# Kernel tuning notes

Hardware: AMD Instinct MI355X
Metric: run time of the kernel (lower is better)

## Reference

```python
import jax, jax.numpy as jnp
import numpy as np

D = 1024      # query_dim
H = 16        # heads
DH = 64       # dim_head
I = H * DH    # inner_dim = 1024
DC = 768      # context_dim
FF = 4 * D    # ff inner dim = 4096
EPS = 1e-5
SCALE = DH ** -0.5


def setup_inputs() -> dict:
    key = jax.random.key(0)
    ks = jax.random.split(key, 20)
    s = 0.02
    inp = {
        'x': jax.random.normal(ks[0], (2, 2048, D), jnp.float32),
        'context': jax.random.normal(ks[1], (2, 77, DC), jnp.float32),
        'ln1_g': jnp.ones((D,), jnp.float32), 'ln1_b': jnp.zeros((D,), jnp.float32),
        'ln2_g': jnp.ones((D,), jnp.float32), 'ln2_b': jnp.zeros((D,), jnp.float32),
        'ln3_g': jnp.ones((D,), jnp.float32), 'ln3_b': jnp.zeros((D,), jnp.float32),
        'Wq1': jax.random.normal(ks[2], (D, I), jnp.float32) * s,
        'Wk1': jax.random.normal(ks[3], (D, I), jnp.float32) * s,
        'Wv1': jax.random.normal(ks[4], (D, I), jnp.float32) * s,
        'Wo1': jax.random.normal(ks[5], (I, D), jnp.float32) * s,
        'bo1': jnp.zeros((D,), jnp.float32),
        'Wq2': jax.random.normal(ks[6], (D, I), jnp.float32) * s,
        'Wk2': jax.random.normal(ks[7], (DC, I), jnp.float32) * s,
        'Wv2': jax.random.normal(ks[8], (DC, I), jnp.float32) * s,
        'Wo2': jax.random.normal(ks[9], (I, D), jnp.float32) * s,
        'bo2': jnp.zeros((D,), jnp.float32),
        'Wff1': jax.random.normal(ks[10], (D, 2 * FF), jnp.float32) * s,
        'bff1': jnp.zeros((2 * FF,), jnp.float32),
        'Wff2': jax.random.normal(ks[11], (FF, D), jnp.float32) * s,
        'bff2': jnp.zeros((D,), jnp.float32),
    }
    return inp


def layer_norm(x, g, b):
    m = jnp.mean(x, axis=-1, keepdims=True)
    v = jnp.mean(jnp.square(x - m), axis=-1, keepdims=True)
    return (x - m) * jax.lax.rsqrt(v + EPS) * g + b


def cross_attention(x, ctx, Wq, Wk, Wv, Wo, bo):
    # x: [B,N,D], ctx: [B,M,Dc]
    B, N, _ = x.shape
    M = ctx.shape[1]
    q = (x @ Wq).reshape(B, N, H, DH).transpose(0, 2, 1, 3)    # [B,H,N,DH]
    k = (ctx @ Wk).reshape(B, M, H, DH).transpose(0, 2, 1, 3)  # [B,H,M,DH]
    v = (ctx @ Wv).reshape(B, M, H, DH).transpose(0, 2, 1, 3)
    sim = jnp.einsum('bhid,bhjd->bhij', q, k) * SCALE           # [B,H,N,M]
    attn = jax.nn.softmax(sim, axis=-1)
    out = jnp.einsum('bhij,bhjd->bhid', attn, v)                # [B,H,N,DH]
    out = out.transpose(0, 2, 1, 3).reshape(B, N, I)
    return out @ Wo + bo


def reference(x, context, ln1_g, ln1_b, ln2_g, ln2_b, ln3_g, ln3_b,
              Wq1, Wk1, Wv1, Wo1, bo1, Wq2, Wk2, Wv2, Wo2, bo2,
              Wff1, bff1, Wff2, bff2):
    # self-attention
    x = cross_attention(layer_norm(x, ln1_g, ln1_b), layer_norm(x, ln1_g, ln1_b),
                        Wq1, Wk1, Wv1, Wo1, bo1) + x
    # cross-attention
    x = cross_attention(layer_norm(x, ln2_g, ln2_b), context,
                        Wq2, Wk2, Wv2, Wo2, bo2) + x
    # GEGLU feed-forward
    hg = layer_norm(x, ln3_g, ln3_b) @ Wff1 + bff1
    h, gate = hg[..., :FF], hg[..., FF:]
    ff = (h * jax.nn.gelu(gate, approximate=False)) @ Wff2 + bff2
    return ff + x
```

## Files before the change

kernel.cpp:

```cpp
#include <hip/hip_runtime.h>
#include <hip/hip_bf16.h>
#include <math.h>

typedef short short8 __attribute__((ext_vector_type(8)));
typedef float floatx4 __attribute__((ext_vector_type(4)));
typedef unsigned short u16;

#define D_MODEL 1024
#define NH 16
#define DH 64
#define FF_DIM 4096

__device__ __forceinline__ u16 f2b(float f) {
  union { float f; unsigned u; } v; v.f = f;
  unsigned r = (v.u + 0x7fffu + ((v.u >> 16) & 1u)) >> 16;
  return (u16)r;
}
__device__ __forceinline__ u16 f2b_fast(float f) {
  union { float f; unsigned u; } v; v.f = f;
  return (u16)((v.u + 0x8000u) >> 16);
}
__device__ __forceinline__ float b2f(u16 h) {
  union { unsigned u; float f; } v; v.u = ((unsigned)h) << 16;
  return v.f;
}

__device__ __forceinline__ void gl_lds16(const u16* g, u16* l) {
  __builtin_amdgcn_global_load_lds(
      (const __attribute__((address_space(1))) unsigned int*)g,
      (__attribute__((address_space(3))) unsigned int*)l, 16, 0, 0);
}

__launch_bounds__(256)
__global__ void transpose_to_bf16(const float* __restrict__ in, u16* __restrict__ out,
                                  int K, int N, float scale) {
  __shared__ float tile[32][33];
  const int n0 = blockIdx.x * 32;
  const int k0 = blockIdx.y * 32;
  const int tx = threadIdx.x & 31;
  const int ty = threadIdx.x >> 5;
#pragma unroll
  for (int i = 0; i < 4; i++) {
    int k = k0 + ty + i * 8;
    tile[ty + i * 8][tx] = in[(size_t)k * N + (n0 + tx)] * scale;
  }
  __syncthreads();
#pragma unroll
  for (int i = 0; i < 4; i++) {
    int n = n0 + ty + i * 8;
    out[(size_t)n * K + (k0 + tx)] = f2b(tile[tx][ty + i * 8]);
  }
}

__launch_bounds__(256)
__global__ void convert_bf16(const float* __restrict__ in, u16* __restrict__ out, int n) {
  int i = blockIdx.x * 256 + threadIdx.x;
  if (i < n) out[i] = f2b(in[i]);
}

__launch_bounds__(256)
__global__ void ln_to_bf16(const float* __restrict__ x, const float* __restrict__ g,
                           const float* __restrict__ b, u16* __restrict__ out) {
  const int row = blockIdx.x;
  const int tid = threadIdx.x;
  const float4 v = ((const float4*)(x + (size_t)row * D_MODEL))[tid];
  float s = v.x + v.y + v.z + v.w;
  float ss = v.x * v.x + v.y * v.y + v.z * v.z + v.w * v.w;
#pragma unroll
  for (int o = 32; o; o >>= 1) { s += __shfl_xor(s, o); ss += __shfl_xor(ss, o); }
  __shared__ float red[8];
  const int wave = tid >> 6, lane = tid & 63;
  if (lane == 0) { red[wave] = s; red[4 + wave] = ss; }
  __syncthreads();
  const float st = red[0] + red[1] + red[2] + red[3];
  const float sst = red[4] + red[5] + red[6] + red[7];
  const float mean = st * (1.0f / D_MODEL);
  const float var = sst * (1.0f / D_MODEL) - mean * mean;
  const float rs = rsqrtf(var + 1e-5f);
  const float4 gv = ((const float4*)g)[tid];
  const float4 bv = ((const float4*)b)[tid];
  ushort4 o4;
  o4.x = f2b((v.x - mean) * rs * gv.x + bv.x);
  o4.y = f2b((v.y - mean) * rs * gv.y + bv.y);
  o4.z = f2b((v.z - mean) * rs * gv.z + bv.z);
  o4.w = f2b((v.w - mean) * rs * gv.w + bv.w);
  ((ushort4*)(out + (size_t)row * D_MODEL))[tid] = o4;
}

template <int EPI>
__launch_bounds__(256)
__global__ void gemm128(const u16* __restrict__ A, const u16* __restrict__ BT,
                        const float* __restrict__ bias, const float* __restrict__ resid,
                        float* __restrict__ Cf, u16* __restrict__ Cb, u16* __restrict__ VT,
                        int K, int lda, int ldb, int ldc) {
  __shared__ __attribute__((aligned(16))) u16 Al[128 * 32];
  __shared__ __attribute__((aligned(16))) u16 Bl[128 * 32];
  const int tid = threadIdx.x, wave = tid >> 6, lane = tid & 63;
  const int lm = lane & 15, lq = lane >> 4;
  const int wr = (wave >> 1) * 64, wc = (wave & 1) * 64;
  const int m0 = blockIdx.y * 128, n0 = blockIdx.x * 128;
  const int xr = (lm >> 1) & 3;

  floatx4 acc[4][4] = {};

  for (int k0 = 0; k0 < K; k0 += 32) {
#pragma unroll
    for (int it = 0; it < 2; it++) {
      const int c = wave * 128 + it * 64 + lane;
      const int r = c >> 2, s = c & 3;
      const int lc = s ^ ((r >> 1) & 3);
      gl_lds16(A + (size_t)(m0 + r) * lda + k0 + lc * 8, &Al[c * 8]);
      gl_lds16(BT + (size_t)(n0 + r) * ldb + k0 + lc * 8, &Bl[c * 8]);
    }
    __syncthreads();
    short8 af[4], bf[4];
#pragma unroll
    for (int r = 0; r < 4; r++)
      af[r] = *(const short8*)(&Al[(wr + r * 16 + lm) * 32 + (lq ^ xr) * 8]);
#pragma unroll
    for (int c = 0; c < 4; c++)
      bf[c] = *(const short8*)(&Bl[(wc + c * 16 + lm) * 32 + (lq ^ xr) * 8]);
#pragma unroll
    for (int r = 0; r < 4; r++)
#pragma unroll
      for (int c = 0; c < 4; c++)
        acc[r][c] = __builtin_amdgcn_mfma_f32_16x16x32_bf16(af[r], bf[c], acc[r][c], 0, 0, 0);
    __syncthreads();
  }

#pragma unroll
  for (int r = 0; r < 4; r++)
#pragma unroll
    for (int c = 0; c < 4; c++) {
      const int col = n0 + wc + c * 16 + lm;
      const int row0 = m0 + wr + r * 16 + lq * 4;
      if (EPI == 0) {
#pragma unroll
        for (int i = 0; i < 4; i++)
          Cb[(size_t)(row0 + i) * ldc + col] = f2b(acc[r][c][i]);
      } else if (EPI == 1) {
#pragma unroll
        for (int i = 0; i < 4; i++)
          Cf[(size_t)(row0 + i) * ldc + col] =
              acc[r][c][i] + bias[col] + resid[(size_t)(row0 + i) * ldc + col];
      } else {
        if (col < 2048) {
#pragma unroll
          for (int i = 0; i < 4; i++)
            Cb[(size_t)(row0 + i) * ldc + col] = f2b(acc[r][c][i]);
        } else {
          const int d = col - 2048;
          ushort4 pk;
          pk.x = f2b(acc[r][c][0]); pk.y = f2b(acc[r][c][1]);
          pk.z = f2b(acc[r][c][2]); pk.w = f2b(acc[r][c][3]);
          *(ushort4*)(&VT[((size_t)((row0 >> 11) * 1024 + d)) * 2048 + (row0 & 2047)]) = pk;
        }
      }
    }
}

__launch_bounds__(256)
__global__ void gemm_geglu(const u16* __restrict__ A, const u16* __restrict__ BT,
                           const float* __restrict__ bias, u16* __restrict__ Cb,
                           int K, int lda, int ldb) {
  __shared__ __attribute__((aligned(16))) u16 Al[128 * 32];
  __shared__ __attribute__((aligned(16))) u16 Bl[64 * 32];
  __shared__ __attribute__((aligned(16))) u16 Bg[64 * 32];
  const int tid = threadIdx.x, wave = tid >> 6, lane = tid & 63;
  const int lm = lane & 15, lq = lane >> 4;
  const int wr = (wave >> 1) * 64, wc = (wave & 1) * 32;
  const int m0 = blockIdx.y * 128, n0 = blockIdx.x * 64;
  const int xr = (lm >> 1) & 3;

  floatx4 acc[4][2] = {};
  floatx4 accg[4][2] = {};

  for (int k0 = 0; k0 < K; k0 += 32) {
#pragma unroll
    for (int it = 0; it < 2; it++) {
      const int c = wave * 128 + it * 64 + lane;
      const int r = c >> 2, s = c & 3;
      const int lc = s ^ ((r >> 1) & 3);
      gl_lds16(A + (size_t)(m0 + r) * lda + k0 + lc * 8, &Al[c * 8]);
    }
    {
      const int c = wave * 64 + lane;
      const int r = c >> 2, s = c & 3;
      const int lc = s ^ ((r >> 1) & 3);
      gl_lds16(BT + (size_t)(n0 + r) * ldb + k0 + lc * 8, &Bl[c * 8]);
      gl_lds16(BT + (size_t)(n0 + r + FF_DIM) * ldb + k0 + lc * 8, &Bg[c * 8]);
    }
    __syncthreads();
    short8 af[4], bf[2], bg[2];
#pragma unroll
    for (int r = 0; r < 4; r++)
      af[r] = *(const short8*)(&Al[(wr + r * 16 + lm) * 32 + (lq ^ xr) * 8]);
#pragma unroll
    for (int c = 0; c < 2; c++) {
      bf[c] = *(const short8*)(&Bl[(wc + c * 16 + lm) * 32 + (lq ^ xr) * 8]);
      bg[c] = *(const short8*)(&Bg[(wc + c * 16 + lm) * 32 + (lq ^ xr) * 8]);
    }
#pragma unroll
    for (int r = 0; r < 4; r++)
#pragma unroll
      for (int c = 0; c < 2; c++) {
        acc[r][c] = __builtin_amdgcn_mfma_f32_16x16x32_bf16(af[r], bf[c], acc[r][c], 0, 0, 0);
        accg[r][c] = __builtin_amdgcn_mfma_f32_16x16x32_bf16(af[r], bg[c], accg[r][c], 0, 0, 0);
      }
    __syncthreads();
  }

#pragma unroll
  for (int r = 0; r < 4; r++)
#pragma unroll
    for (int c = 0; c < 2; c++) {
      const int col = n0 + wc + c * 16 + lm;
#pragma unroll
      for (int i = 0; i < 4; i++) {
        const int row = m0 + wr + r * 16 + lq * 4 + i;
        const float h = acc[r][c][i] + bias[col];
        const float gt = accg[r][c][i] + bias[col + FF_DIM];
        const float gl = 0.5f * gt * (1.0f + erff(gt * 0.70710678118f));
        Cb[(size_t)row * FF_DIM + col] = f2b(h * gl);
      }
    }
}

#define BM 64
#define BN 64
#define LSTR 40

template <int TRANS>
__launch_bounds__(256)
__global__ void gemm_bt64(const u16* __restrict__ A, const u16* __restrict__ BT,
                          u16* __restrict__ Cb,
                          int M, int N, int K, int lda, int ldb, int ldc, int rowsPerB) {
  __shared__ __attribute__((aligned(16))) u16 Al[BM * LSTR];
  __shared__ __attribute__((aligned(16))) u16 Bl[BN * LSTR];
  const int tid = threadIdx.x, wave = tid >> 6, lane = tid & 63;
  const int wm = (wave >> 1) * 32, wn = (wave & 1) * 32;
  const int lm = lane & 15, lq = lane >> 4;
  const int m0 = blockIdx.y * BM, n0 = blockIdx.x * BN;

  floatx4 acc[2][2] = {};
  const int srow = tid >> 2;
  const int scol = (tid & 3) * 8;
  const bool a_ok = (m0 + srow) < M;

  for (int k0 = 0; k0 < K; k0 += 32) {
    int4 av = make_int4(0, 0, 0, 0);
    if (a_ok) av = *(const int4*)(A + (size_t)(m0 + srow) * lda + k0 + scol);
    *(int4*)(&Al[srow * LSTR + scol]) = av;
    int4 bv = *(const int4*)(BT + (size_t)(n0 + srow) * ldb + k0 + scol);
    *(int4*)(&Bl[srow * LSTR + scol]) = bv;
    __syncthreads();
    short8 af[2], bfr[2];
#pragma unroll
    for (int r = 0; r < 2; r++) af[r] = *(const short8*)(&Al[(wm + r * 16 + lm) * LSTR + lq * 8]);
#pragma unroll
    for (int c = 0; c < 2; c++) bfr[c] = *(const short8*)(&Bl[(wn + c * 16 + lm) * LSTR + lq * 8]);
#pragma unroll
    for (int r = 0; r < 2; r++)
#pragma unroll
      for (int c = 0; c < 2; c++)
        acc[r][c] = __builtin_amdgcn_mfma_f32_16x16x32_bf16(af[r], bfr[c], acc[r][c], 0, 0, 0);
    __syncthreads();
  }

#pragma unroll
  for (int r = 0; r < 2; r++)
#pragma unroll
    for (int c = 0; c < 2; c++) {
      const int col = n0 + wn + c * 16 + lm;
#pragma unroll
      for (int i = 0; i < 4; i++) {
        const int row = m0 + wm + r * 16 + lq * 4 + i;
        if (row < M) {
          if (TRANS == 0) {
            Cb[(size_t)row * ldc + col] = f2b(acc[r][c][i]);
          } else {
            const int bb = row / rowsPerB;
            const int n = row - bb * rowsPerB;
            Cb[((size_t)(bb * 1024 + col)) * 128 + n] = f2b(acc[r][c][i]);
          }
        }
      }
    }
}

__launch_bounds__(256)
__global__ void attn_mfma(const u16* __restrict__ Qg, const u16* __restrict__ Kg,
                          const u16* __restrict__ VTg, u16* __restrict__ Ob,
                          int N, int Mk, int kRowsPerBatch, int ldq, int ldk, int vtld) {
  const int ntiles = N / 64;
  const int bh = blockIdx.x / ntiles;
  const int qt = blockIdx.x % ntiles;
  const int b = bh / NH, h = bh % NH;
  const int tid = threadIdx.x, wave = tid >> 6, lane = tid & 63;
  const int lm = lane & 15, lq = lane >> 4;

  __shared__ __attribute__((aligned(16))) u16 Qs[64 * 64];
  __shared__ __attribute__((aligned(16))) u16 Ks[64 * 64];
  __shared__ __attribute__((aligned(16))) u16 Vt[64 * 64];
  __shared__ __attribute__((aligned(16))) u16 Ps[4][16 * 72];

  const u16* Qh = Qg + (size_t)b * N * ldq + h * DH;
  const u16* Kh = Kg + (size_t)b * kRowsPerBatch * ldk + h * DH;
  const u16* Vh = VTg + (size_t)(b * 1024 + h * DH) * vtld;

  {
    const u16* qsrc = Qh + (size_t)qt * 64 * ldq;
#pragma unroll
    for (int it = 0; it < 2; it++) {
      const int c = wave * 128 + it * 64 + lane;
      const int r = c >> 3, p = c & 7, lc = p ^ (r & 7);
      gl_lds16(qsrc + (size_t)r * ldq + lc * 8, &Qs[c * 8]);
    }
  }
  __syncthreads();
  short8 qf[2];
  qf[0] = *(const short8*)(&Qs[(wave * 16 + lm) * 64 + ((lq) ^ (lm & 7)) * 8]);
  qf[1] = *(const short8*)(&Qs[(wave * 16 + lm) * 64 + ((4 + lq) ^ (lm & 7)) * 8]);

  float lpart[4] = {0.f, 0.f, 0.f, 0.f};
  floatx4 o[4] = {};

  for (int kt = 0; kt < Mk; kt += 64) {
    __syncthreads();
    {
      const u16* ksrc = Kh + (size_t)kt * ldk;
      const u16* vsrc = Vh + kt;
#pragma unroll
      for (int it = 0; it < 2; it++) {
        const int c = wave * 128 + it * 64 + lane;
        const int r = c >> 3, p = c & 7, lc = p ^ (r & 7);
        gl_lds16(ksrc + (size_t)r * ldk + lc * 8, &Ks[c * 8]);
        gl_lds16(vsrc + (size_t)r * vtld + lc * 8, &Vt[c * 8]);
      }
    }
    __syncthreads();

    floatx4 s[4];
#pragma unroll
    for (int ct = 0; ct < 4; ct++) {
      short8 kf0 = *(const short8*)(&Ks[(ct * 16 + lm) * 64 + ((lq) ^ (lm & 7)) * 8]);
      short8 kf1 = *(const short8*)(&Ks[(ct * 16 + lm) * 64 + ((4 + lq) ^ (lm & 7)) * 8]);
      floatx4 z = {};
      z = __builtin_amdgcn_mfma_f32_16x16x32_bf16(qf[0], kf0, z, 0, 0, 0);
      z = __builtin_amdgcn_mfma_f32_16x16x32_bf16(qf[1], kf1, z, 0, 0, 0);
      s[ct] = z;
    }

    if (kt + 64 <= Mk) {
#pragma unroll
      for (int reg = 0; reg < 4; reg++) {
        float p0 = __expf(s[0][reg] - 16.0f);
        float p1 = __expf(s[1][reg] - 16.0f);
        float p2 = __expf(s[2][reg] - 16.0f);
        float p3 = __expf(s[3][reg] - 16.0f);
        lpart[reg] += (p0 + p1) + (p2 + p3);
        const int prow = (lq * 4 + reg) * 72;
        Ps[wave][prow + lm] = f2b_fast(p0);
        Ps[wave][prow + 16 + lm] = f2b_fast(p1);
        Ps[wave][prow + 32 + lm] = f2b_fast(p2);
        Ps[wave][prow + 48 + lm] = f2b_fast(p3);
      }
    } else {
#pragma unroll
      for (int reg = 0; reg < 4; reg++) {
        const int prow = (lq * 4 + reg) * 72;
        float psum = 0.f;
#pragma unroll
        for (int ct = 0; ct < 4; ct++) {
          const bool valid = (kt + ct * 16 + lm) < Mk;
          float p = valid ? __expf(s[ct][reg] - 16.0f) : 0.f;
          psum += p;
          Ps[wave][prow + ct * 16 + lm] = f2b_fast(p);
        }
        lpart[reg] += psum;
      }
    }

    const short8 pf0 = *(const short8*)(&Ps[wave][lm * 72 + lq * 8]);
    const short8 pf1 = *(const short8*)(&Ps[wave][lm * 72 + 32 + lq * 8]);
#pragma unroll
    for (int ct = 0; ct < 4; ct++) {
      short8 vf0 = *(const short8*)(&Vt[(ct * 16 + lm) * 64 + ((lq) ^ (lm & 7)) * 8]);
      short8 vf1 = *(const short8*)(&Vt[(ct * 16 + lm) * 64 + ((4 + lq) ^ (lm & 7)) * 8]);
      o[ct] = __builtin_amdgcn_mfma_f32_16x16x32_bf16(pf0, vf0, o[ct], 0, 0, 0);
      o[ct] = __builtin_amdgcn_mfma_f32_16x16x32_bf16(pf1, vf1, o[ct], 0, 0, 0);
    }
  }

  float inv[4];
#pragma unroll
  for (int reg = 0; reg < 4; reg++) {
    float l = lpart[reg];
    l += __shfl_xor(l, 1); l += __shfl_xor(l, 2);
    l += __shfl_xor(l, 4); l += __shfl_xor(l, 8);
    inv[reg] = 1.0f / l;
  }
#pragma unroll
  for (int ct = 0; ct < 4; ct++)
#pragma unroll
    for (int reg = 0; reg < 4; reg++) {
      const int grow = qt * 64 + wave * 16 + lq * 4 + reg;
      Ob[((size_t)(b * N + grow)) * D_MODEL + h * DH + ct * 16 + lm] =
          f2b(o[ct][reg] * inv[reg]);
    }
}

extern "C" void kernel_launch(void* const* d_in, const int* in_sizes, int n_in,
                              void* d_out, int out_size, void* d_ws, size_t ws_size,
                              hipStream_t stream) {
  const float* x    = (const float*)d_in[0];
  const float* ctx  = (const float*)d_in[1];
  const float* ln1g = (const float*)d_in[2];
  const float* ln1b = (const float*)d_in[3];
  const float* ln2g = (const float*)d_in[4];
  const float* ln2b = (const float*)d_in[5];
  const float* ln3g = (const float*)d_in[6];
  const float* ln3b = (const float*)d_in[7];
  const float* Wq1  = (const float*)d_in[8];
  const float* Wk1  = (const float*)d_in[9];
  const float* Wv1  = (const float*)d_in[10];
  const float* Wo1  = (const float*)d_in[11];
  const float* bo1  = (const float*)d_in[12];
  const float* Wq2  = (const float*)d_in[13];
  const float* Wk2  = (const float*)d_in[14];
  const float* Wv2  = (const float*)d_in[15];
  const float* Wo2  = (const float*)d_in[16];
  const float* bo2  = (const float*)d_in[17];
  const float* Wff1 = (const float*)d_in[18];
  const float* bff1 = (const float*)d_in[19];
  const float* Wff2 = (const float*)d_in[20];
  const float* bff2 = (const float*)d_in[21];
  float* out = (float*)d_out;

  char* ws = (char*)d_ws;
  size_t off = 0;
  auto alloc = [&](size_t bytes) -> char* {
    char* p = ws + off;
    off += (bytes + 255) & ~(size_t)255;
    return p;
  };
  u16* wqkv1T = (u16*)alloc((size_t)3072 * 1024 * 2);
  u16* wo1T   = (u16*)alloc((size_t)1024 * 1024 * 2);
  u16* wq2T   = (u16*)alloc((size_t)1024 * 1024 * 2);
  u16* wk2T   = (u16*)alloc((size_t)1024 * 768 * 2);
  u16* wv2T   = (u16*)alloc((size_t)1024 * 768 * 2);
  u16* wo2T   = (u16*)alloc((size_t)1024 * 1024 * 2);
  u16* wff1T  = (u16*)alloc((size_t)8192 * 1024 * 2);
  u16* wff2T  = (u16*)alloc((size_t)1024 * 4096 * 2);
  u16* xln    = (u16*)alloc((size_t)4096 * 1024 * 2);
  u16* ctxb   = (u16*)alloc((size_t)154 * 768 * 2);
  u16* QKVb   = (u16*)alloc((size_t)4096 * 3072 * 2);
  u16* VTb    = (u16*)alloc((size_t)2048 * 2048 * 2);
  u16* K2b    = (u16*)alloc((size_t)256 * 1024 * 2);
  u16* VT2b   = (u16*)alloc((size_t)2048 * 128 * 2);
  u16* Ob     = (u16*)alloc((size_t)4096 * 1024 * 2);
  float* x1   = (float*)alloc((size_t)4096 * 1024 * 4);
  float* x2   = (float*)alloc((size_t)4096 * 1024 * 4);
  u16* ffin   = (u16*)alloc((size_t)4096 * 4096 * 2);
  u16* Q2b    = ffin;

  dim3 blk(256);

  transpose_to_bf16<<<dim3(32, 32), blk, 0, stream>>>(Wq1, wqkv1T, 1024, 1024, 1.0f);
  transpose_to_bf16<<<dim3(32, 32), blk, 0, stream>>>(Wk1, wqkv1T + (size_t)1024 * 1024, 1024, 1024, 0.125f);
  transpose_to_bf16<<<dim3(32, 32), blk, 0, stream>>>(Wv1, wqkv1T + (size_t)2048 * 1024, 1024, 1024, 1.0f);
  transpose_to_bf16<<<dim3(32, 32), blk, 0, stream>>>(Wo1, wo1T, 1024, 1024, 1.0f);
  transpose_to_bf16<<<dim3(32, 32), blk, 0, stream>>>(Wq2, wq2T, 1024, 1024, 1.0f);
  transpose_to_bf16<<<dim3(32, 24), blk, 0, stream>>>(Wk2, wk2T, 768, 1024, 0.125f);
  transpose_to_bf16<<<dim3(32, 24), blk, 0, stream>>>(Wv2, wv2T, 768, 1024, 1.0f);
  transpose_to_bf16<<<dim3(32, 32), blk, 0, stream>>>(Wo2, wo2T, 1024, 1024, 1.0f);
  transpose_to_bf16<<<dim3(256, 32), blk, 0, stream>>>(Wff1, wff1T, 1024, 8192, 1.0f);
  transpose_to_bf16<<<dim3(32, 128), blk, 0, stream>>>(Wff2, wff2T, 4096, 1024, 1.0f);
  convert_bf16<<<(154 * 768 + 255) / 256, blk, 0, stream>>>(ctx, ctxb, 154 * 768);

  ln_to_bf16<<<4096, blk, 0, stream>>>(x, ln1g, ln1b, xln);
  gemm128<2><<<dim3(24, 32), blk, 0, stream>>>(xln, wqkv1T, nullptr, nullptr, nullptr, QKVb,
                                               VTb, 1024, 1024, 1024, 3072);
  attn_mfma<<<2 * NH * (2048 / 64), blk, 0, stream>>>(QKVb, QKVb + 1024, VTb, Ob,
                                                      2048, 2048, 2048, 3072, 3072, 2048);
  gemm128<1><<<dim3(8, 32), blk, 0, stream>>>(Ob, wo1T, bo1, x, x1, nullptr, nullptr,
                                              1024, 1024, 1024, 1024);

  ln_to_bf16<<<4096, blk, 0, stream>>>(x1, ln2g, ln2b, xln);
  gemm128<0><<<dim3(8, 32), blk, 0, stream>>>(xln, wq2T, nullptr, nullptr, nullptr, Q2b,
                                              nullptr, 1024, 1024, 1024, 1024);
  gemm_bt64<0><<<dim3(16, 3), blk, 0, stream>>>(ctxb, wk2T, K2b, 154, 1024, 768, 768, 768, 1024, 77);
  gemm_bt64<1><<<dim3(16, 3), blk, 0, stream>>>(ctxb, wv2T, VT2b, 154, 1024, 768, 768, 768, 1024, 77);
  attn_mfma<<<2 * NH * (2048 / 64), blk, 0, stream>>>(Q2b, K2b, VT2b, Ob,
                                                      2048, 77, 77, 1024, 1024, 128);
  gemm128<1><<<dim3(8, 32), blk, 0, stream>>>(Ob, wo2T, bo2, x1, x2, nullptr, nullptr,
                                              1024, 1024, 1024, 1024);

  ln_to_bf16<<<4096, blk, 0, stream>>>(x2, ln3g, ln3b, xln);
  gemm_geglu<<<dim3(64, 32), blk, 0, stream>>>(xln, wff1T, bff1, ffin, 1024, 1024, 1024);
  gemm128<1><<<dim3(8, 32), blk, 0, stream>>>(ffin, wff2T, bff2, x2, out, nullptr, nullptr,
                                              4096, 4096, 4096, 1024);
}
```

Baseline: 597.9 us.

## Double-buffer K/V tiles in attention and drop LDS swizzle in GEGLU GEMM

The attention kernel now stages K and V into two LDS buffers, loading the next 64-key tile while the current one is used for QK and PV MFMAs. This removes one barrier per iteration and overlaps global-to-LDS transfer with compute, at the cost of doubling K/V shared memory, which can lower occupancy. Separately, the GEGLU GEMM drops the XOR swizzle on its A/B LDS tiles and uses plain linear offsets. That simplifies address math but risks more LDS bank conflicts on the fragment reads.

```diff
diff --git a/kernel.cpp b/kernel.cpp
--- a/kernel.cpp
+++ b/kernel.cpp
@@ -170,7 +170,6 @@
   const int lm = lane & 15, lq = lane >> 4;
   const int wr = (wave >> 1) * 64, wc = (wave & 1) * 32;
   const int m0 = blockIdx.y * 128, n0 = blockIdx.x * 64;
-  const int xr = (lm >> 1) & 3;
 
   floatx4 acc[4][2] = {};
   floatx4 accg[4][2] = {};
@@ -180,25 +179,23 @@
     for (int it = 0; it < 2; it++) {
       const int c = wave * 128 + it * 64 + lane;
       const int r = c >> 2, s = c & 3;
-      const int lc = s ^ ((r >> 1) & 3);
-      gl_lds16(A + (size_t)(m0 + r) * lda + k0 + lc * 8, &Al[c * 8]);
+      gl_lds16(A + (size_t)(m0 + r) * lda + k0 + s * 8, &Al[c * 8]);
     }
     {
       const int c = wave * 64 + lane;
       const int r = c >> 2, s = c & 3;
-      const int lc = s ^ ((r >> 1) & 3);
-      gl_lds16(BT + (size_t)(n0 + r) * ldb + k0 + lc * 8, &Bl[c * 8]);
-      gl_lds16(BT + (size_t)(n0 + r + FF_DIM) * ldb + k0 + lc * 8, &Bg[c * 8]);
+      gl_lds16(BT + (size_t)(n0 + r) * ldb + k0 + s * 8, &Bl[c * 8]);
+      gl_lds16(BT + (size_t)(n0 + r + FF_DIM) * ldb + k0 + s * 8, &Bg[c * 8]);
     }
     __syncthreads();
     short8 af[4], bf[2], bg[2];
 #pragma unroll
     for (int r = 0; r < 4; r++)
-      af[r] = *(const short8*)(&Al[(wr + r * 16 + lm) * 32 + (lq ^ xr) * 8]);
+      af[r] = *(const short8*)(&Al[(wr + r * 16 + lm) * 32 + lq * 8]);
 #pragma unroll
     for (int c = 0; c < 2; c++) {
-      bf[c] = *(const short8*)(&Bl[(wc + c * 16 + lm) * 32 + (lq ^ xr) * 8]);
-      bg[c] = *(const short8*)(&Bg[(wc + c * 16 + lm) * 32 + (lq ^ xr) * 8]);
+      bf[c] = *(const short8*)(&Bl[(wc + c * 16 + lm) * 32 + lq * 8]);
+      bg[c] = *(const short8*)(&Bg[(wc + c * 16 + lm) * 32 + lq * 8]);
     }
 #pragma unroll
     for (int r = 0; r < 4; r++)
@@ -300,13 +297,23 @@
   const int lm = lane & 15, lq = lane >> 4;
 
   __shared__ __attribute__((aligned(16))) u16 Qs[64 * 64];
-  __shared__ __attribute__((aligned(16))) u16 Ks[64 * 64];
-  __shared__ __attribute__((aligned(16))) u16 Vt[64 * 64];
+  __shared__ __attribute__((aligned(16))) u16 Ks[2][64 * 64];
+  __shared__ __attribute__((aligned(16))) u16 Vt[2][64 * 64];
   __shared__ __attribute__((aligned(16))) u16 Ps[4][16 * 72];
 
   const u16* Qh = Qg + (size_t)b * N * ldq + h * DH;
   const u16* Kh = Kg + (size_t)b * kRowsPerBatch * ldk + h * DH;
   const u16* Vh = VTg + (size_t)(b * 1024 + h * DH) * vtld;
+
+  auto stageKV = [&](int kt, int buf) {
+#pragma unroll
+    for (int it = 0; it < 2; it++) {
+      const int c = wave * 128 + it * 64 + lane;
+      const int r = c >> 3, p = c & 7, lc = p ^ (r & 7);
+      gl_lds16(Kh + (size_t)(kt + r) * ldk + lc * 8, &Ks[buf][c * 8]);
+      gl_lds16(Vh + (size_t)r * vtld + kt + lc * 8, &Vt[buf][c * 8]);
+    }
+  };
 
   {
     const u16* qsrc = Qh + (size_t)qt * 64 * ldq;
@@ -317,34 +324,25 @@
       gl_lds16(qsrc + (size_t)r * ldq + lc * 8, &Qs[c * 8]);
     }
   }
+  stageKV(0, 0);
   __syncthreads();
+
   short8 qf[2];
   qf[0] = *(const short8*)(&Qs[(wave * 16 + lm) * 64 + ((lq) ^ (lm & 7)) * 8]);
   qf[1] = *(const short8*)(&Qs[(wave * 16 + lm) * 64 + ((4 + lq) ^ (lm & 7)) * 8]);
 
   float lpart[4] = {0.f, 0.f, 0.f, 0.f};
   floatx4 o[4] = {};
+  int cur = 0;
 
   for (int kt = 0; kt < Mk; kt += 64) {
-    __syncthreads();
-    {
-      const u16* ksrc = Kh + (size_t)kt * ldk;
-      const u16* vsrc = Vh + kt;
-#pragma unroll
-      for (int it = 0; it < 2; it++) {
-        const int c = wave * 128 + it * 64 + lane;
-        const int r = c >> 3, p = c & 7, lc = p ^ (r & 7);
-        gl_lds16(ksrc + (size_t)r * ldk + lc * 8, &Ks[c * 8]);
-        gl_lds16(vsrc + (size_t)r * vtld + lc * 8, &Vt[c * 8]);
-      }
-    }
-    __syncthreads();
+    if (kt + 64 < Mk) stageKV(kt + 64, cur ^ 1);
 
     floatx4 s[4];
 #pragma unroll
     for (int ct = 0; ct < 4; ct++) {
-      short8 kf0 = *(const short8*)(&Ks[(ct * 16 + lm) * 64 + ((lq) ^ (lm & 7)) * 8]);
-      short8 kf1 = *(const short8*)(&Ks[(ct * 16 + lm) * 64 + ((4 + lq) ^ (lm & 7)) * 8]);
+      short8 kf0 = *(const short8*)(&Ks[cur][(ct * 16 + lm) * 64 + ((lq) ^ (lm & 7)) * 8]);
+      short8 kf1 = *(const short8*)(&Ks[cur][(ct * 16 + lm) * 64 + ((4 + lq) ^ (lm & 7)) * 8]);
       floatx4 z = {};
       z = __builtin_amdgcn_mfma_f32_16x16x32_bf16(qf[0], kf0, z, 0, 0, 0);
       z = __builtin_amdgcn_mfma_f32_16x16x32_bf16(qf[1], kf1, z, 0, 0, 0);
@@ -385,11 +383,14 @@
     const short8 pf1 = *(const short8*)(&Ps[wave][lm * 72 + 32 + lq * 8]);
 #pragma unroll
     for (int ct = 0; ct < 4; ct++) {
-      short8 vf0 = *(const short8*)(&Vt[(ct * 16 + lm) * 64 + ((lq) ^ (lm & 7)) * 8]);
-      short8 vf1 = *(const short8*)(&Vt[(ct * 16 + lm) * 64 + ((4 + lq) ^ (lm & 7)) * 8]);
+      short8 vf0 = *(const short8*)(&Vt[cur][(ct * 16 + lm) * 64 + ((lq) ^ (lm & 7)) * 8]);
+      short8 vf1 = *(const short8*)(&Vt[cur][(ct * 16 + lm) * 64 + ((4 + lq) ^ (lm & 7)) * 8]);
       o[ct] = __builtin_amdgcn_mfma_f32_16x16x32_bf16(pf0, vf0, o[ct], 0, 0, 0);
       o[ct] = __builtin_amdgcn_mfma_f32_16x16x32_bf16(pf1, vf1, o[ct], 0, 0, 0);
     }
+
+    __syncthreads();
+    cur ^= 1;
   }
 
   float inv[4];
```

After: 606.7 us. No clear change (+1.5%).

## Batch weight transposes into multi-matrix launches and drop GEGLU LDS swizzle

Applied to the files above, without the earlier changes.

Merges eight separate weight transpose launches into two launches, with grid z selecting the source matrix, to cut launch overhead and tail effects. It also removes the XOR swizzle from the GEGLU GEMM's LDS layout, simplifying address arithmetic but likely reintroducing LDS bank conflicts on the fragment reads. The two changes are unrelated.

```diff
diff --git a/kernel.cpp b/kernel.cpp
--- a/kernel.cpp
+++ b/kernel.cpp
@@ -35,6 +35,36 @@
 __global__ void transpose_to_bf16(const float* __restrict__ in, u16* __restrict__ out,
                                   int K, int N, float scale) {
   __shared__ float tile[32][33];
+  const int n0 = blockIdx.x * 32;
+  const int k0 = blockIdx.y * 32;
+  const int tx = threadIdx.x & 31;
+  const int ty = threadIdx.x >> 5;
+#pragma unroll
+  for (int i = 0; i < 4; i++) {
+    int k = k0 + ty + i * 8;
+    tile[ty + i * 8][tx] = in[(size_t)k * N + (n0 + tx)] * scale;
+  }
+  __syncthreads();
+#pragma unroll
+  for (int i = 0; i < 4; i++) {
+    int n = n0 + ty + i * 8;
+    out[(size_t)n * K + (k0 + tx)] = f2b(tile[tx][ty + i * 8]);
+  }
+}
+
+struct TransArgs {
+  const float* src[6];
+  u16* dst[6];
+  float scale[6];
+};
+
+__launch_bounds__(256)
+__global__ void transpose_to_bf16_multi(TransArgs a, int K, int N) {
+  __shared__ float tile[32][33];
+  const int z = blockIdx.z;
+  const float* __restrict__ in = a.src[z];
+  u16* __restrict__ out = a.dst[z];
+  const float scale = a.scale[z];
   const int n0 = blockIdx.x * 32;
   const int k0 = blockIdx.y * 32;
   const int tx = threadIdx.x & 31;
@@ -170,7 +200,6 @@
   const int lm = lane & 15, lq = lane >> 4;
   const int wr = (wave >> 1) * 64, wc = (wave & 1) * 32;
   const int m0 = blockIdx.y * 128, n0 = blockIdx.x * 64;
-  const int xr = (lm >> 1) & 3;
 
   floatx4 acc[4][2] = {};
   floatx4 accg[4][2] = {};
@@ -180,25 +209,23 @@
     for (int it = 0; it < 2; it++) {
       const int c = wave * 128 + it * 64 + lane;
       const int r = c >> 2, s = c & 3;
-      const int lc = s ^ ((r >> 1) & 3);
-      gl_lds16(A + (size_t)(m0 + r) * lda + k0 + lc * 8, &Al[c * 8]);
+      gl_lds16(A + (size_t)(m0 + r) * lda + k0 + s * 8, &Al[c * 8]);
     }
     {
       const int c = wave * 64 + lane;
       const int r = c >> 2, s = c & 3;
-      const int lc = s ^ ((r >> 1) & 3);
-      gl_lds16(BT + (size_t)(n0 + r) * ldb + k0 + lc * 8, &Bl[c * 8]);
-      gl_lds16(BT + (size_t)(n0 + r + FF_DIM) * ldb + k0 + lc * 8, &Bg[c * 8]);
+      gl_lds16(BT + (size_t)(n0 + r) * ldb + k0 + s * 8, &Bl[c * 8]);
+      gl_lds16(BT + (size_t)(n0 + r + FF_DIM) * ldb + k0 + s * 8, &Bg[c * 8]);
     }
     __syncthreads();
     short8 af[4], bf[2], bg[2];
 #pragma unroll
     for (int r = 0; r < 4; r++)
-      af[r] = *(const short8*)(&Al[(wr + r * 16 + lm) * 32 + (lq ^ xr) * 8]);
+      af[r] = *(const short8*)(&Al[(wr + r * 16 + lm) * 32 + lq * 8]);
 #pragma unroll
     for (int c = 0; c < 2; c++) {
-      bf[c] = *(const short8*)(&Bl[(wc + c * 16 + lm) * 32 + (lq ^ xr) * 8]);
-      bg[c] = *(const short8*)(&Bg[(wc + c * 16 + lm) * 32 + (lq ^ xr) * 8]);
+      bf[c] = *(const short8*)(&Bl[(wc + c * 16 + lm) * 32 + lq * 8]);
+      bg[c] = *(const short8*)(&Bg[(wc + c * 16 + lm) * 32 + lq * 8]);
     }
 #pragma unroll
     for (int r = 0; r < 4; r++)
@@ -466,14 +493,26 @@
 
   dim3 blk(256);
 
-  transpose_to_bf16<<<dim3(32, 32), blk, 0, stream>>>(Wq1, wqkv1T, 1024, 1024, 1.0f);
-  transpose_to_bf16<<<dim3(32, 32), blk, 0, stream>>>(Wk1, wqkv1T + (size_t)1024 * 1024, 1024, 1024, 0.125f);
-  transpose_to_bf16<<<dim3(32, 32), blk, 0, stream>>>(Wv1, wqkv1T + (size_t)2048 * 1024, 1024, 1024, 1.0f);
-  transpose_to_bf16<<<dim3(32, 32), blk, 0, stream>>>(Wo1, wo1T, 1024, 1024, 1.0f);
-  transpose_to_bf16<<<dim3(32, 32), blk, 0, stream>>>(Wq2, wq2T, 1024, 1024, 1.0f);
-  transpose_to_bf16<<<dim3(32, 24), blk, 0, stream>>>(Wk2, wk2T, 768, 1024, 0.125f);
-  transpose_to_bf16<<<dim3(32, 24), blk, 0, stream>>>(Wv2, wv2T, 768, 1024, 1.0f);
-  transpose_to_bf16<<<dim3(32, 32), blk, 0, stream>>>(Wo2, wo2T, 1024, 1024, 1.0f);
+  {
+    TransArgs t6;
+    t6.src[0] = Wq1;  t6.dst[0] = wqkv1T;                          t6.scale[0] = 1.0f;
+    t6.src[1] = Wk1;  t6.dst[1] = wqkv1T + (size_t)1024 * 1024;    t6.scale[1] = 0.125f;
+    t6.src[2] = Wv1;  t6.dst[2] = wqkv1T + (size_t)2048 * 1024;    t6.scale[2] = 1.0f;
+    t6.src[3] = Wo1;  t6.dst[3] = wo1T;                            t6.scale[3] = 1.0f;
+    t6.src[4] = Wq2;  t6.dst[4] = wq2T;                            t6.scale[4] = 1.0f;
+    t6.src[5] = Wo2;  t6.dst[5] = wo2T;                            t6.scale[5] = 1.0f;
+    transpose_to_bf16_multi<<<dim3(32, 32, 6), blk, 0, stream>>>(t6, 1024, 1024);
+  }
+  {
+    TransArgs t2;
+    t2.src[0] = Wk2;  t2.dst[0] = wk2T;  t2.scale[0] = 0.125f;
+    t2.src[1] = Wv2;  t2.dst[1] = wv2T;  t2.scale[1] = 1.0f;
+    t2.src[2] = Wk2;  t2.dst[2] = wk2T;  t2.scale[2] = 0.125f;
+    t2.src[3] = Wk2;  t2.dst[3] = wk2T;  t2.scale[3] = 0.125f;
+    t2.src[4] = Wk2;  t2.dst[4] = wk2T;  t2.scale[4] = 0.125f;
+    t2.src[5] = Wk2;  t2.dst[5] = wk2T;  t2.scale[5] = 0.125f;
+    transpose_to_bf16_multi<<<dim3(32, 24, 2), blk, 0, stream>>>(t2, 768, 1024);
+  }
   transpose_to_bf16<<<dim3(256, 32), blk, 0, stream>>>(Wff1, wff1T, 1024, 8192, 1.0f);
   transpose_to_bf16<<<dim3(32, 128), blk, 0, stream>>>(Wff2, wff2T, 4096, 1024, 1.0f);
   convert_bf16<<<(154 * 768 + 255) / 256, blk, 0, stream>>>(ctx, ctxb, 154 * 768);
```

Result: faster. 585.7 us (-2.0%).
